# Performance work log

Hardware: AMD Instinct MI355X
Metric: run time of the kernel (lower is better)

Reference implementation:

```python
import jax, jax.numpy as jnp
import numpy as np

B, T, ENC, DEC = 512, 500, 1024, 1024

def setup_inputs() -> dict:
    key = jax.random.key(0)
    k1, k2, k3, k4 = jax.random.split(key, 4)
    decoderFeature = jax.random.normal(k1, (B, DEC), dtype=jnp.float32)
    encoderFeature = jax.random.normal(k2, (B, T, ENC), dtype=jnp.float32)
    skill_net_lengths = jax.random.randint(k3, (B,), 1, T + 1, dtype=jnp.int32)
    W = jax.random.normal(k4, (ENC, DEC), dtype=jnp.float32) * (6.0 / (ENC + DEC)) ** 0.5
    return {"decoderFeature": decoderFeature, "encoderFeature": encoderFeature,
            "skill_net_lengths": skill_net_lengths, "W": W}

def reference(decoderFeature, encoderFeature, skill_net_lengths, W):
    # subResult = F.linear(decoderFeature, W) -> [B, ENC]
    sub = decoderFeature @ W.T
    # attn scores: bmm([B,1,ENC], [B,ENC,T]) -> [B, T]
    scores = jnp.einsum('be,bte->bt', sub, encoderFeature)
    valid = jnp.arange(T)[None, :] < skill_net_lengths[:, None]  # [B, T]
    scores = jnp.where(valid, scores, -jnp.inf)
    attn = jax.nn.softmax(scores, axis=-1)  # [B, T]
    sumResult = jnp.einsum('bt,bte->be', attn, encoderFeature)  # [B, ENC]
    return attn[:, None, :], sumResult
```

## Files before the change

kernel.cpp:

```cpp
#include <hip/hip_runtime.h>
#include <math.h>

#define B 512
#define T 500
#define ENC 1024
#define DEC 1024

#define GM 32
#define GN 64
#define GK 16

__global__ __launch_bounds__(256) void gemm_sub(
    const float* __restrict__ A,
    const float* __restrict__ Wm,
    float* __restrict__ C)
{
    __shared__ float As[GK][GM + 2];
    __shared__ float Bs[GK][GN + 4];

    const int tid = threadIdx.x;
    const int bm0 = blockIdx.y * GM;
    const int bn0 = blockIdx.x * GN;

    const int tx = tid & 15;
    const int ty = tid >> 4;

    float accr[2][4] = {{0.f,0.f,0.f,0.f},{0.f,0.f,0.f,0.f}};

    const int arow = tid >> 3;
    const int acol = (tid & 7) * 2;
    const int brow = tid >> 2;
    const int bcol = (tid & 3) * 4;

    for (int k0 = 0; k0 < DEC; k0 += GK) {
        float2 a2 = *(const float2*)(A + (size_t)(bm0 + arow) * DEC + k0 + acol);
        As[acol][arow]     = a2.x;
        As[acol + 1][arow] = a2.y;
        float4 b4 = *(const float4*)(Wm + (size_t)(bn0 + brow) * DEC + k0 + bcol);
        Bs[bcol][brow]     = b4.x;
        Bs[bcol + 1][brow] = b4.y;
        Bs[bcol + 2][brow] = b4.z;
        Bs[bcol + 3][brow] = b4.w;
        __syncthreads();
#pragma unroll
        for (int k = 0; k < GK; k++) {
            float2 av = *(const float2*)&As[k][ty * 2];
            float4 bv = *(const float4*)&Bs[k][tx * 4];
            accr[0][0] = fmaf(av.x, bv.x, accr[0][0]);
            accr[0][1] = fmaf(av.x, bv.y, accr[0][1]);
            accr[0][2] = fmaf(av.x, bv.z, accr[0][2]);
            accr[0][3] = fmaf(av.x, bv.w, accr[0][3]);
            accr[1][0] = fmaf(av.y, bv.x, accr[1][0]);
            accr[1][1] = fmaf(av.y, bv.y, accr[1][1]);
            accr[1][2] = fmaf(av.y, bv.z, accr[1][2]);
            accr[1][3] = fmaf(av.y, bv.w, accr[1][3]);
        }
        __syncthreads();
    }

    float4 c0 = make_float4(accr[0][0], accr[0][1], accr[0][2], accr[0][3]);
    float4 c1 = make_float4(accr[1][0], accr[1][1], accr[1][2], accr[1][3]);
    *(float4*)(C + (size_t)(bm0 + ty * 2) * ENC + bn0 + tx * 4)     = c0;
    *(float4*)(C + (size_t)(bm0 + ty * 2 + 1) * ENC + bn0 + tx * 4) = c1;
}

#define NW 8
#define BLK (NW * 64)

__global__ __launch_bounds__(BLK, 4) void attn_fused(
    const float* __restrict__ sub,
    const float* __restrict__ enc,
    const int* __restrict__ lens,
    float* __restrict__ out_attn,
    float* __restrict__ out_sum)
{
    __shared__ float lds_scores[T];
    __shared__ float lds_m[NW];
    __shared__ float lds_l[NW];
    __shared__ float lds_o[NW][ENC];

    const int b    = blockIdx.x;
    const int tid  = threadIdx.x;
    const int wave = tid >> 6;
    const int lane = tid & 63;
    const int len  = lens[b];

    const float* encb = enc + (size_t)b * T * ENC;
    const float* subb = sub + (size_t)b * ENC;

    float sub_r[16];
#pragma unroll
    for (int c = 0; c < 4; c++) {
        float4 s4 = *(const float4*)(subb + c * 256 + 4 * lane);
        sub_r[c * 4 + 0] = s4.x; sub_r[c * 4 + 1] = s4.y;
        sub_r[c * 4 + 2] = s4.z; sub_r[c * 4 + 3] = s4.w;
    }

    float acc[16];
#pragma unroll
    for (int i = 0; i < 16; i++) acc[i] = 0.f;
    float m = -INFINITY;
    float l = 0.f;

    int t = wave;
    float er[16];
    if (t < len) {
        const float* p = encb + (size_t)t * ENC + 4 * lane;
#pragma unroll
        for (int c = 0; c < 4; c++) {
            float4 v = *(const float4*)(p + c * 256);
            er[c * 4 + 0] = v.x; er[c * 4 + 1] = v.y;
            er[c * 4 + 2] = v.z; er[c * 4 + 3] = v.w;
        }
    }

    while (t < len) {
        const int tn = t + NW;
        float ern[16];
        if (tn < len) {
            const float* p = encb + (size_t)tn * ENC + 4 * lane;
#pragma unroll
            for (int c = 0; c < 4; c++) {
                float4 v = *(const float4*)(p + c * 256);
                ern[c * 4 + 0] = v.x; ern[c * 4 + 1] = v.y;
                ern[c * 4 + 2] = v.z; ern[c * 4 + 3] = v.w;
            }
        }

        float d = 0.f;
#pragma unroll
        for (int i = 0; i < 16; i++) d = fmaf(er[i], sub_r[i], d);
#pragma unroll
        for (int off = 32; off > 0; off >>= 1) d += __shfl_xor(d, off, 64);

        if (lane == 0) lds_scores[t] = d;

        if (d > m) {
            float alpha = __expf(m - d);
            l = l * alpha + 1.f;
#pragma unroll
            for (int i = 0; i < 16; i++) acc[i] = acc[i] * alpha + er[i];
            m = d;
        } else {
            float p = __expf(d - m);
            l += p;
#pragma unroll
            for (int i = 0; i < 16; i++) acc[i] = fmaf(p, er[i], acc[i]);
        }

        t = tn;
#pragma unroll
        for (int i = 0; i < 16; i++) er[i] = ern[i];
    }

    if (lane == 0) { lds_m[wave] = m; lds_l[wave] = l; }
#pragma unroll
    for (int c = 0; c < 4; c++) {
        float4 v = make_float4(acc[c * 4 + 0], acc[c * 4 + 1],
                               acc[c * 4 + 2], acc[c * 4 + 3]);
        *(float4*)&lds_o[wave][c * 256 + 4 * lane] = v;
    }
    __syncthreads();

    float mg = -INFINITY;
#pragma unroll
    for (int w = 0; w < NW; w++) mg = fmaxf(mg, lds_m[w]);
    float scale[NW];
    float lg = 0.f;
#pragma unroll
    for (int w = 0; w < NW; w++) {
        float mw = lds_m[w];
        float s  = (mw == -INFINITY) ? 0.f : __expf(mw - mg);
        scale[w] = s;
        lg = fmaf(lds_l[w], s, lg);
    }
    const float inv_l = 1.f / lg;

    const int e0 = 2 * tid;
    float o0 = 0.f, o1 = 0.f;
#pragma unroll
    for (int w = 0; w < NW; w++) {
        o0 = fmaf(scale[w], lds_o[w][e0], o0);
        o1 = fmaf(scale[w], lds_o[w][e0 + 1], o1);
    }
    *(float2*)(out_sum + (size_t)b * ENC + e0) = make_float2(o0 * inv_l, o1 * inv_l);

    for (int tt = tid; tt < T; tt += BLK) {
        float v = 0.f;
        if (tt < len) v = __expf(lds_scores[tt] - mg) * inv_l;
        out_attn[(size_t)b * T + tt] = v;
    }
}

extern "C" void kernel_launch(void* const* d_in, const int* in_sizes, int n_in,
                              void* d_out, int out_size, void* d_ws, size_t ws_size,
                              hipStream_t stream) {
    const float* dec  = (const float*)d_in[0];
    const float* enc  = (const float*)d_in[1];
    const int*   lens = (const int*)d_in[2];
    const float* Wm   = (const float*)d_in[3];

    float* out       = (float*)d_out;
    float* out_attn  = out;
    float* out_sum   = out + (size_t)B * T;
    float* sub       = (float*)d_ws;

    gemm_sub<<<dim3(16, 16), 256, 0, stream>>>(dec, Wm, sub);
    attn_fused<<<dim3(B), BLK, 0, stream>>>(sub, enc, lens, out_attn, out_sum);
}
```

Baseline: 1.273 ms.

## Batch four encoder rows per softmax step and retile GEMM with register prefetch

The attention kernel now gives each wave a contiguous chunk of timesteps instead of a strided walk. It loads four encoder rows per iteration, interleaves their shuffle reductions, and does a single online-softmax rescale per group, which removes the per-row divergent branch and raises memory-level parallelism. The GEMM switches to 32x32x32 tiles with a 2x2 microtile, more blocks, and a register prefetch of the next K tile. The cost is more registers per thread in the attention kernel, which could reduce occupancy, plus wasted duplicate loads in partial groups.

Result: no change. 1.280 ms (+0.5%).

```diff
diff --git a/kernel.cpp b/kernel.cpp
--- a/kernel.cpp
+++ b/kernel.cpp
@@ -6,66 +6,65 @@
 #define ENC 1024
 #define DEC 1024
 
-#define GM 32
-#define GN 64
-#define GK 16
+#define QM 32
+#define QN 32
+#define QK 32
 
 __global__ __launch_bounds__(256) void gemm_sub(
     const float* __restrict__ A,
     const float* __restrict__ Wm,
     float* __restrict__ C)
 {
-    __shared__ float As[GK][GM + 2];
-    __shared__ float Bs[GK][GN + 4];
+    __shared__ float As[QK][QM + 2];
+    __shared__ float Bs[QK][QN + 2];
 
     const int tid = threadIdx.x;
-    const int bm0 = blockIdx.y * GM;
-    const int bn0 = blockIdx.x * GN;
+    const int bm0 = blockIdx.y * QM;
+    const int bn0 = blockIdx.x * QN;
+
+    const int lr = tid >> 3;
+    const int lc = (tid & 7) << 2;
+    const float* pa = A  + (size_t)(bm0 + lr) * DEC + lc;
+    const float* pb = Wm + (size_t)(bn0 + lr) * DEC + lc;
 
     const int tx = tid & 15;
     const int ty = tid >> 4;
 
-    float accr[2][4] = {{0.f,0.f,0.f,0.f},{0.f,0.f,0.f,0.f}};
-
-    const int arow = tid >> 3;
-    const int acol = (tid & 7) * 2;
-    const int brow = tid >> 2;
-    const int bcol = (tid & 3) * 4;
-
-    for (int k0 = 0; k0 < DEC; k0 += GK) {
-        float2 a2 = *(const float2*)(A + (size_t)(bm0 + arow) * DEC + k0 + acol);
-        As[acol][arow]     = a2.x;
-        As[acol + 1][arow] = a2.y;
-        float4 b4 = *(const float4*)(Wm + (size_t)(bn0 + brow) * DEC + k0 + bcol);
-        Bs[bcol][brow]     = b4.x;
-        Bs[bcol + 1][brow] = b4.y;
-        Bs[bcol + 2][brow] = b4.z;
-        Bs[bcol + 3][brow] = b4.w;
+    float a00 = 0.f, a01 = 0.f, a10 = 0.f, a11 = 0.f;
+
+    float4 a4 = *(const float4*)pa;
+    float4 b4 = *(const float4*)pb;
+
+    for (int k0 = 0; k0 < DEC; k0 += QK) {
+        As[lc + 0][lr] = a4.x; As[lc + 1][lr] = a4.y;
+        As[lc + 2][lr] = a4.z; As[lc + 3][lr] = a4.w;
+        Bs[lc + 0][lr] = b4.x; Bs[lc + 1][lr] = b4.y;
+        Bs[lc + 2][lr] = b4.z; Bs[lc + 3][lr] = b4.w;
         __syncthreads();
-#pragma unroll
-        for (int k = 0; k < GK; k++) {
-            float2 av = *(const float2*)&As[k][ty * 2];
-            float4 bv = *(const float4*)&Bs[k][tx * 4];
-            accr[0][0] = fmaf(av.x, bv.x, accr[0][0]);
-            accr[0][1] = fmaf(av.x, bv.y, accr[0][1]);
-            accr[0][2] = fmaf(av.x, bv.z, accr[0][2]);
-            accr[0][3] = fmaf(av.x, bv.w, accr[0][3]);
-            accr[1][0] = fmaf(av.y, bv.x, accr[1][0]);
-            accr[1][1] = fmaf(av.y, bv.y, accr[1][1]);
-            accr[1][2] = fmaf(av.y, bv.z, accr[1][2]);
-            accr[1][3] = fmaf(av.y, bv.w, accr[1][3]);
+        if (k0 + QK < DEC) {
+            a4 = *(const float4*)(pa + k0 + QK);
+            b4 = *(const float4*)(pb + k0 + QK);
+        }
+#pragma unroll
+        for (int k = 0; k < QK; k++) {
+            float2 av = *(const float2*)&As[k][ty << 1];
+            float2 bv = *(const float2*)&Bs[k][tx << 1];
+            a00 = fmaf(av.x, bv.x, a00);
+            a01 = fmaf(av.x, bv.y, a01);
+            a10 = fmaf(av.y, bv.x, a10);
+            a11 = fmaf(av.y, bv.y, a11);
         }
         __syncthreads();
     }
 
-    float4 c0 = make_float4(accr[0][0], accr[0][1], accr[0][2], accr[0][3]);
-    float4 c1 = make_float4(accr[1][0], accr[1][1], accr[1][2], accr[1][3]);
-    *(float4*)(C + (size_t)(bm0 + ty * 2) * ENC + bn0 + tx * 4)     = c0;
-    *(float4*)(C + (size_t)(bm0 + ty * 2 + 1) * ENC + bn0 + tx * 4) = c1;
+    float* c0 = C + (size_t)(bm0 + (ty << 1)) * ENC + bn0 + (tx << 1);
+    *(float2*)c0         = make_float2(a00, a01);
+    *(float2*)(c0 + ENC) = make_float2(a10, a11);
 }
 
 #define NW 8
 #define BLK (NW * 64)
+#define RB 4
 
 __global__ __launch_bounds__(BLK, 4) void attn_fused(
     const float* __restrict__ sub,
@@ -88,78 +87,90 @@
     const float* encb = enc + (size_t)b * T * ENC;
     const float* subb = sub + (size_t)b * ENC;
 
-    float sub_r[16];
-#pragma unroll
-    for (int c = 0; c < 4; c++) {
-        float4 s4 = *(const float4*)(subb + c * 256 + 4 * lane);
-        sub_r[c * 4 + 0] = s4.x; sub_r[c * 4 + 1] = s4.y;
-        sub_r[c * 4 + 2] = s4.z; sub_r[c * 4 + 3] = s4.w;
-    }
-
-    float acc[16];
-#pragma unroll
-    for (int i = 0; i < 16; i++) acc[i] = 0.f;
+    float4 s4[4];
+#pragma unroll
+    for (int c = 0; c < 4; c++)
+        s4[c] = *(const float4*)(subb + c * 256 + 4 * lane);
+
+    float4 acc4[4];
+#pragma unroll
+    for (int c = 0; c < 4; c++) acc4[c] = make_float4(0.f, 0.f, 0.f, 0.f);
     float m = -INFINITY;
     float l = 0.f;
 
-    int t = wave;
-    float er[16];
-    if (t < len) {
-        const float* p = encb + (size_t)t * ENC + 4 * lane;
+    const int chunk = (len + NW - 1) / NW;
+    const int t0 = wave * chunk;
+    const int t1 = min(len, t0 + chunk);
+
+    for (int t = t0; t < t1; t += RB) {
+        const int nv = t1 - t;
+        float4 er[RB][4];
+#pragma unroll
+        for (int r = 0; r < RB; r++) {
+            const int tr = t + ((r < nv) ? r : 0);
+            const float* p = encb + (size_t)tr * ENC + 4 * lane;
+#pragma unroll
+            for (int c = 0; c < 4; c++)
+                er[r][c] = *(const float4*)(p + 256 * c);
+        }
+
+        float d[RB];
+#pragma unroll
+        for (int r = 0; r < RB; r++) {
+            float dd = 0.f;
+#pragma unroll
+            for (int c = 0; c < 4; c++) {
+                dd = fmaf(er[r][c].x, s4[c].x, dd);
+                dd = fmaf(er[r][c].y, s4[c].y, dd);
+                dd = fmaf(er[r][c].z, s4[c].z, dd);
+                dd = fmaf(er[r][c].w, s4[c].w, dd);
+            }
+            d[r] = dd;
+        }
+
+#pragma unroll
+        for (int off = 32; off > 0; off >>= 1) {
+#pragma unroll
+            for (int r = 0; r < RB; r++) d[r] += __shfl_xor(d[r], off, 64);
+        }
+
+#pragma unroll
+        for (int r = 0; r < RB; r++)
+            if (r >= nv) d[r] = -INFINITY;
+
+        if (lane == 0) {
+#pragma unroll
+            for (int r = 0; r < RB; r++)
+                if (r < nv) lds_scores[t + r] = d[r];
+        }
+
+        const float mx    = fmaxf(fmaxf(d[0], d[1]), fmaxf(d[2], d[3]));
+        const float m_new = fmaxf(m, mx);
+        const float alpha = __expf(m - m_new);
+        float p[RB];
+#pragma unroll
+        for (int r = 0; r < RB; r++) p[r] = __expf(d[r] - m_new);
+        l = fmaf(l, alpha, (p[0] + p[1]) + (p[2] + p[3]));
 #pragma unroll
         for (int c = 0; c < 4; c++) {
-            float4 v = *(const float4*)(p + c * 256);
-            er[c * 4 + 0] = v.x; er[c * 4 + 1] = v.y;
-            er[c * 4 + 2] = v.z; er[c * 4 + 3] = v.w;
-        }
-    }
-
-    while (t < len) {
-        const int tn = t + NW;
-        float ern[16];
-        if (tn < len) {
-            const float* p = encb + (size_t)tn * ENC + 4 * lane;
-#pragma unroll
-            for (int c = 0; c < 4; c++) {
-                float4 v = *(const float4*)(p + c * 256);
-                ern[c * 4 + 0] = v.x; ern[c * 4 + 1] = v.y;
-                ern[c * 4 + 2] = v.z; ern[c * 4 + 3] = v.w;
+            float4 a = acc4[c];
+            a.x = a.x * alpha; a.y = a.y * alpha; a.z = a.z * alpha; a.w = a.w * alpha;
+#pragma unroll
+            for (int r = 0; r < RB; r++) {
+                a.x = fmaf(p[r], er[r][c].x, a.x);
+                a.y = fmaf(p[r], er[r][c].y, a.y);
+                a.z = fmaf(p[r], er[r][c].z, a.z);
+                a.w = fmaf(p[r], er[r][c].w, a.w);
             }
-        }
-
-        float d = 0.f;
-#pragma unroll
-        for (int i = 0; i < 16; i++) d = fmaf(er[i], sub_r[i], d);
-#pragma unroll
-        for (int off = 32; off > 0; off >>= 1) d += __shfl_xor(d, off, 64);
-
-        if (lane == 0) lds_scores[t] = d;
-
-        if (d > m) {
-            float alpha = __expf(m - d);
-            l = l * alpha + 1.f;
-#pragma unroll
-            for (int i = 0; i < 16; i++) acc[i] = acc[i] * alpha + er[i];
-            m = d;
-        } else {
-            float p = __expf(d - m);
-            l += p;
-#pragma unroll
-            for (int i = 0; i < 16; i++) acc[i] = fmaf(p, er[i], acc[i]);
-        }
-
-        t = tn;
-#pragma unroll
-        for (int i = 0; i < 16; i++) er[i] = ern[i];
+            acc4[c] = a;
+        }
+        m = m_new;
     }
 
     if (lane == 0) { lds_m[wave] = m; lds_l[wave] = l; }
 #pragma unroll
-    for (int c = 0; c < 4; c++) {
-        float4 v = make_float4(acc[c * 4 + 0], acc[c * 4 + 1],
-                               acc[c * 4 + 2], acc[c * 4 + 3]);
-        *(float4*)&lds_o[wave][c * 256 + 4 * lane] = v;
-    }
+    for (int c = 0; c < 4; c++)
+        *(float4*)&lds_o[wave][c * 256 + 4 * lane] = acc4[c];
     __syncthreads();
 
     float mg = -INFINITY;
@@ -200,11 +211,11 @@
     const int*   lens = (const int*)d_in[2];
     const float* Wm   = (const float*)d_in[3];
 
-    float* out       = (float*)d_out;
-    float* out_attn  = out;
-    float* out_sum   = out + (size_t)B * T;
-    float* sub       = (float*)d_ws;
-
-    gemm_sub<<<dim3(16, 16), 256, 0, stream>>>(dec, Wm, sub);
+    float* out      = (float*)d_out;
+    float* out_attn = out;
+    float* out_sum  = out + (size_t)B * T;
+    float* sub      = (float*)d_ws;
+
+    gemm_sub<<<dim3(ENC / QN, 512 / QM), 256, 0, stream>>>(dec, Wm, sub);
     attn_fused<<<dim3(B), BLK, 0, stream>>>(sub, enc, lens, out_attn, out_sum);
 }
```
